# Optimization experiments

Measured on AMD Instinct MI355X. Metric: run time of the kernel, lower is better.

Reference implementation:

```python
import jax, jax.numpy as jnp
import numpy as np


def setup_inputs() -> dict:
    key = jax.random.key(0)
    ks = jax.random.split(key, 5)
    B, T, H, L = 32, 1024, 512, 2
    scale = 1.0 / np.sqrt(H)
    x = jax.random.normal(ks[0], (B, T, H), dtype=jnp.float32)
    Wi = jax.random.normal(ks[1], (L, 4 * H, H), dtype=jnp.float32) * scale
    bi = jax.random.normal(ks[2], (L, 4 * H), dtype=jnp.float32) * scale
    Ws = jax.random.normal(ks[3], (L, 4 * H, H), dtype=jnp.float32) * scale
    # state_linearity bias: zeros except forget slice [H:2H] = 1 (reset_parameters)
    bs = jnp.zeros((L, 4 * H), dtype=jnp.float32)
    bs = bs.at[:, H:2 * H].set(1.0)
    return {"x": x, "Wi": Wi, "bi": bi, "Ws": Ws, "bs": bs}


def reference(x, Wi, bi, Ws, bs):
    # x: [B,T,H]; Wi/Ws: [L,4C,H]; bi/bs: [L,4C]; here C == H (no projection layer)
    B, T, H = x.shape
    L = Wi.shape[0]
    C = H

    def step(carry, x_t):
        h, c = carry  # each [L,B,C]
        inp = x_t  # [B,H]
        new_h, new_c = [], []
        for j in range(L):
            z = inp @ Wi[j].T + bi[j] + h[j] @ Ws[j].T + bs[j]  # [B,4C]
            ig = jax.nn.sigmoid(z[:, 0 * C:1 * C])
            fg = jax.nn.sigmoid(z[:, 1 * C:2 * C])
            gg = jnp.tanh(z[:, 2 * C:3 * C])
            og = jax.nn.sigmoid(z[:, 3 * C:4 * C])
            c_j = ig * gg + fg * c[j]
            h_j = og * jnp.tanh(c_j) + inp  # residual skip connection
            inp = h_j
            new_h.append(h_j)
            new_c.append(c_j)
        return (jnp.stack(new_h), jnp.stack(new_c)), inp

    h0 = jnp.zeros((L, B, C), dtype=x.dtype)
    c0 = jnp.zeros((L, B, C), dtype=x.dtype)
    (h_f, c_f), ys = jax.lax.scan(step, (h0, c0), jnp.swapaxes(x, 0, 1))
    out = jnp.swapaxes(ys, 0, 1)  # [B,T,H]
    # final states as (B, L, H) matching module layout
    return out, jnp.swapaxes(h_f, 0, 1), jnp.swapaxes(c_f, 0, 1)
```

## Files before the change

### kernel.cpp

```cpp
#include <hip/hip_runtime.h>


typedef unsigned int uint32;
typedef unsigned short ushort;

constexpr int B = 32, T = 1024, H = 512, NL = 2;
constexpr int KTOT = 2 * H;
constexpr int BH   = B * H;
constexpr size_t BTH = (size_t)B * T * H;
constexpr size_t BLH = (size_t)B * NL * H;

using bf16x8  = __attribute__((ext_vector_type(8))) short;
using floatx4 = __attribute__((ext_vector_type(4))) float;
using uint4v  = __attribute__((ext_vector_type(4))) uint32;

__device__ __forceinline__ float frcp(float x) { return __builtin_amdgcn_rcpf(x); }
__device__ __forceinline__ float sigm(float v) { return frcp(1.0f + __expf(-v)); }
__device__ __forceinline__ float tanh_fast(float v) {
    return 1.0f - 2.0f * frcp(1.0f + __expf(2.0f * v));
}

__device__ __forceinline__ ushort f2bf(float f) {
    uint32 u = __builtin_bit_cast(uint32, f);
    u += 0x7fffu + ((u >> 16) & 1u);
    return (ushort)(u >> 16);
}

__launch_bounds__(512, 1)
__global__ void lstm_persist(const float* __restrict__ x,
                             const float* __restrict__ Wi,
                             const float* __restrict__ bi,
                             const float* __restrict__ Ws,
                             const float* __restrict__ bs,
                             float* __restrict__ out,
                             uint32* __restrict__ ctrl,
                             uint32* __restrict__ h0pk,
                             uint32* __restrict__ h1pk)
{
    extern __shared__ short smem[];
    short* whi = smem;
    short* wlo = smem + 32 * KTOT;
    float* red = (float*)(smem + 64 * KTOT);

    const int wg    = blockIdx.x;
    const int tid   = threadIdx.x;
    const int layer = wg & 1;
    const int rg    = wg >> 1;
    const int chb   = rg * 8;

    for (int i = tid; i < 32 * KTOT; i += 512) {
        const int n = i >> 10, k = i & (KTOT - 1);
        const int g = n >> 3, c = n & 7;
        const int grow = g * H + chb + c;
        const float v = (k < H) ? Wi[((size_t)layer * 4 * H + grow) * H + k]
                                : Ws[((size_t)layer * 4 * H + grow) * H + (k - H)];
        const ushort hb = f2bf(v);
        const float  hf = __builtin_bit_cast(float, (uint32)hb << 16);
        const ushort lb = f2bf(v - hf);
        const int off = (n * 128 + ((k >> 3) ^ n)) * 8 + (k & 7);
        whi[off] = (short)hb;
        wlo[off] = (short)lb;
    }

    const int lane = tid & 63;
    const int w    = tid >> 6;
    const int mt   = w & 1;
    const int kq   = w >> 1;
    const int quad = lane >> 4;
    const int mrow = lane & 15;
    const int bb   = mt * 16 + mrow;
    const int nn   = mrow;

    const int ec = tid & 7, eb = tid >> 3;
    float cs = 0.f;
    float bias_[4] = {0.f, 0.f, 0.f, 0.f};
    if (tid < 256) {
        #pragma unroll
        for (int g = 0; g < 4; ++g) {
            const int grow = g * H + chb + ec;
            bias_[g] = bi[layer * 4 * H + grow] + bs[layer * 4 * H + grow];
        }
    }

    const bool xwave = (layer == 0) && (kq < 2);
    float4 xq[16];
    if (xwave) {
        const float* xb = x + ((size_t)bb * T + 0) * H + kq * 256 + quad * 8;
        #pragma unroll
        for (int st = 0; st < 8; ++st) {
            xq[2 * st]     = *(const float4*)(xb + st * 32);
            xq[2 * st + 1] = *(const float4*)(xb + st * 32 + 4);
        }
    }
    __syncthreads();

    for (int s = 0; s <= T; ++s) {
        const int t = (layer == 0) ? s : s - 1;
        const bool active = (t >= 0 && t < T);

        float resid = 0.f;
        if (active && tid < 256) {
            const int ch = chb + ec;
            if (layer == 0) {
                resid = x[((size_t)eb * T + t) * H + ch];
            } else {
                const uint32 rp = __hip_atomic_load(
                    &h0pk[(size_t)(t & 1) * BH + (size_t)eb * H + ch],
                    __ATOMIC_RELAXED, __HIP_MEMORY_SCOPE_AGENT);
                resid = __builtin_bit_cast(float, rp << 16)
                      + __builtin_bit_cast(float, rp & 0xffff0000u);
            }
        }

        if (active) {
            floatx4 acc0 = {0.f, 0.f, 0.f, 0.f};
            floatx4 acc1 = {0.f, 0.f, 0.f, 0.f};
            floatx4 acc2 = {0.f, 0.f, 0.f, 0.f};
            floatx4 acc3 = {0.f, 0.f, 0.f, 0.f};

            if (xwave) {
                #pragma unroll
                for (int st = 0; st < 8; ++st) {
                    const float4 f0 = xq[2 * st], f1 = xq[2 * st + 1];
                    const float vv[8] = {f0.x, f0.y, f0.z, f0.w, f1.x, f1.y, f1.z, f1.w};
                    bf16x8 ahi, alo;
                    #pragma unroll
                    for (int j = 0; j < 8; ++j) {
                        const ushort hb = f2bf(vv[j]);
                        const float  hf = __builtin_bit_cast(float, (uint32)hb << 16);
                        ahi[j] = (short)hb;
                        alo[j] = (short)f2bf(vv[j] - hf);
                    }
                    const int cb = kq * 32 + st * 4 + quad;
                    const int n1 = 16 + nn;
                    const int woff0 = (nn * 128 + (cb ^ nn)) * 8;
                    const int woff1 = (n1 * 128 + (cb ^ n1)) * 8;
                    const bf16x8 bh0 = *(const bf16x8*)(whi + woff0);
                    const bf16x8 bl0 = *(const bf16x8*)(wlo + woff0);
                    const bf16x8 bh1 = *(const bf16x8*)(whi + woff1);
                    const bf16x8 bl1 = *(const bf16x8*)(wlo + woff1);
                    acc0 = __builtin_amdgcn_mfma_f32_16x16x32_bf16(ahi, bh0, acc0, 0, 0, 0);
                    acc1 = __builtin_amdgcn_mfma_f32_16x16x32_bf16(alo, bh0, acc1, 0, 0, 0);
                    acc1 = __builtin_amdgcn_mfma_f32_16x16x32_bf16(ahi, bl0, acc1, 0, 0, 0);
                    acc2 = __builtin_amdgcn_mfma_f32_16x16x32_bf16(ahi, bh1, acc2, 0, 0, 0);
                    acc3 = __builtin_amdgcn_mfma_f32_16x16x32_bf16(alo, bh1, acc3, 0, 0, 0);
                    acc3 = __builtin_amdgcn_mfma_f32_16x16x32_bf16(ahi, bl1, acc3, 0, 0, 0);
                }
            } else {
                int par, koff;
                const uint32* hbuf;
                if (layer == 0)   { par = (t - 1) & 1; koff = kq * 256 - 512; hbuf = h0pk; }
                else if (kq < 2)  { par = t & 1;       koff = kq * 256;       hbuf = h0pk; }
                else              { par = (t - 1) & 1; koff = kq * 256 - 512; hbuf = h1pk; }
                const uint32* hp = hbuf + (size_t)par * BH + (size_t)bb * H + koff + quad * 8;

                uint4v q0,q1,q2,q3,q4,q5,q6,q7,q8,q9,q10,q11,q12,q13,q14,q15;
                asm volatile(
                    "global_load_dwordx4 %0,  %16, off sc0 sc1\n\t"
                    "global_load_dwordx4 %1,  %16, off offset:16 sc0 sc1\n\t"
                    "global_load_dwordx4 %2,  %16, off offset:128 sc0 sc1\n\t"
                    "global_load_dwordx4 %3,  %16, off offset:144 sc0 sc1\n\t"
                    "global_load_dwordx4 %4,  %16, off offset:256 sc0 sc1\n\t"
                    "global_load_dwordx4 %5,  %16, off offset:272 sc0 sc1\n\t"
                    "global_load_dwordx4 %6,  %16, off offset:384 sc0 sc1\n\t"
                    "global_load_dwordx4 %7,  %16, off offset:400 sc0 sc1\n\t"
                    "global_load_dwordx4 %8,  %16, off offset:512 sc0 sc1\n\t"
                    "global_load_dwordx4 %9,  %16, off offset:528 sc0 sc1\n\t"
                    "global_load_dwordx4 %10, %16, off offset:640 sc0 sc1\n\t"
                    "global_load_dwordx4 %11, %16, off offset:656 sc0 sc1\n\t"
                    "global_load_dwordx4 %12, %16, off offset:768 sc0 sc1\n\t"
                    "global_load_dwordx4 %13, %16, off offset:784 sc0 sc1\n\t"
                    "global_load_dwordx4 %14, %16, off offset:896 sc0 sc1\n\t"
                    "global_load_dwordx4 %15, %16, off offset:912 sc0 sc1\n\t"
                    "s_waitcnt vmcnt(0)"
                    : "=&v"(q0), "=&v"(q1), "=&v"(q2), "=&v"(q3),
                      "=&v"(q4), "=&v"(q5), "=&v"(q6), "=&v"(q7),
                      "=&v"(q8), "=&v"(q9), "=&v"(q10), "=&v"(q11),
                      "=&v"(q12), "=&v"(q13), "=&v"(q14), "=&v"(q15)
                    : "v"(hp)
                    : "memory");
                const uint4v qq[16] = {q0,q1,q2,q3,q4,q5,q6,q7,q8,q9,q10,q11,q12,q13,q14,q15};

                #pragma unroll
                for (int st = 0; st < 8; ++st) {
                    const uint4v ea = qq[2 * st], eb4 = qq[2 * st + 1];
                    uint4v hiw, low;
                    hiw[0] = __builtin_amdgcn_perm(ea[1],  ea[0],  0x05040100u);
                    hiw[1] = __builtin_amdgcn_perm(ea[3],  ea[2],  0x05040100u);
                    hiw[2] = __builtin_amdgcn_perm(eb4[1], eb4[0], 0x05040100u);
                    hiw[3] = __builtin_amdgcn_perm(eb4[3], eb4[2], 0x05040100u);
                    low[0] = __builtin_amdgcn_perm(ea[1],  ea[0],  0x07060302u);
                    low[1] = __builtin_amdgcn_perm(ea[3],  ea[2],  0x07060302u);
                    low[2] = __builtin_amdgcn_perm(eb4[1], eb4[0], 0x07060302u);
                    low[3] = __builtin_amdgcn_perm(eb4[3], eb4[2], 0x07060302u);
                    const bf16x8 ahi = __builtin_bit_cast(bf16x8, hiw);
                    const bf16x8 alo = __builtin_bit_cast(bf16x8, low);
                    const int cb = kq * 32 + st * 4 + quad;
                    const int n1 = 16 + nn;
                    const int woff0 = (nn * 128 + (cb ^ nn)) * 8;
                    const int woff1 = (n1 * 128 + (cb ^ n1)) * 8;
                    const bf16x8 bh0 = *(const bf16x8*)(whi + woff0);
                    const bf16x8 bl0 = *(const bf16x8*)(wlo + woff0);
                    const bf16x8 bh1 = *(const bf16x8*)(whi + woff1);
                    const bf16x8 bl1 = *(const bf16x8*)(wlo + woff1);
                    acc0 = __builtin_amdgcn_mfma_f32_16x16x32_bf16(ahi, bh0, acc0, 0, 0, 0);
                    acc1 = __builtin_amdgcn_mfma_f32_16x16x32_bf16(alo, bh0, acc1, 0, 0, 0);
                    acc1 = __builtin_amdgcn_mfma_f32_16x16x32_bf16(ahi, bl0, acc1, 0, 0, 0);
                    acc2 = __builtin_amdgcn_mfma_f32_16x16x32_bf16(ahi, bh1, acc2, 0, 0, 0);
                    acc3 = __builtin_amdgcn_mfma_f32_16x16x32_bf16(alo, bh1, acc3, 0, 0, 0);
                    acc3 = __builtin_amdgcn_mfma_f32_16x16x32_bf16(ahi, bl1, acc3, 0, 0, 0);
                }
            }
            floatx4 zr0, zr1;
            zr0[0] = acc0[0] + acc1[0]; zr0[1] = acc0[1] + acc1[1];
            zr0[2] = acc0[2] + acc1[2]; zr0[3] = acc0[3] + acc1[3];
            zr1[0] = acc2[0] + acc3[0]; zr1[1] = acc2[1] + acc3[1];
            zr1[2] = acc2[2] + acc3[2]; zr1[3] = acc2[3] + acc3[3];
            *(floatx4*)&red[((w * 2 + 0) * 64 + lane) * 4] = zr0;
            *(floatx4*)&red[((w * 2 + 1) * 64 + lane) * 4] = zr1;
        }
        __syncthreads();

        float hn_s = 0.f;
        if (active && tid < 256) {
            const int m = eb & 15, emt = eb >> 4, q = m >> 2, r = m & 3;
            const int ch = chb + ec;
            float z[4];
            #pragma unroll
            for (int g = 0; g < 4; ++g) {
                const int n = g * 8 + ec;
                const int nt = n >> 4, col = n & 15;
                const int li = q * 16 + col;
                float a = bias_[g];
                #pragma unroll
                for (int kqe = 0; kqe < 4; ++kqe)
                    a += red[((((kqe * 2 + emt) * 2) + nt) * 64 + li) * 4 + r];
                z[g] = a;
            }
            const float ig = sigm(z[0]), fg = sigm(z[1]);
            const float gg = tanh_fast(z[2]), og = sigm(z[3]);
            cs = ig * gg + fg * cs;
            hn_s = og * tanh_fast(cs) + resid;

            const ushort hb = f2bf(hn_s);
            const float  hf = __builtin_bit_cast(float, (uint32)hb << 16);
            const ushort lb = f2bf(hn_s - hf);
            const uint32 pk = (uint32)hb | ((uint32)lb << 16);
            const size_t hidx = (size_t)(t & 1) * BH + (size_t)eb * H + ch;
            if (layer == 0) {
                __hip_atomic_store(&h0pk[hidx], pk, __ATOMIC_RELAXED, __HIP_MEMORY_SCOPE_AGENT);
            } else {
                __hip_atomic_store(&h1pk[hidx], pk, __ATOMIC_RELAXED, __HIP_MEMORY_SCOPE_AGENT);
            }
        }

        __syncthreads();

        if (tid == 448 && s < T) {
            const uint32 e = (uint32)s + 1u;
            const uint32 rr = __hip_atomic_fetch_add(&ctrl[0], 1u, __ATOMIC_RELAXED,
                                                     __HIP_MEMORY_SCOPE_AGENT);
            if (rr == e * 128u - 1u)
                __hip_atomic_store(&ctrl[512], e,
                                   __ATOMIC_RELAXED, __HIP_MEMORY_SCOPE_AGENT);
        }

        if (active && tid < 256) {
            const int ch = chb + ec;
            if (layer == 1)
                out[((size_t)eb * T + t) * H + ch] = hn_s;
            if (t == T - 1) {
                out[BTH + ((size_t)eb * NL + layer) * H + ch] = hn_s;
                out[BTH + BLH + ((size_t)eb * NL + layer) * H + ch] = cs;
            }
        }

        if (s < T) {
            if (xwave && (s + 1) < T) {
                const float* xb = x + ((size_t)bb * T + (s + 1)) * H + kq * 256 + quad * 8;
                #pragma unroll
                for (int st = 0; st < 8; ++st) {
                    xq[2 * st]     = *(const float4*)(xb + st * 32);
                    xq[2 * st + 1] = *(const float4*)(xb + st * 32 + 4);
                }
            }
            const uint32 e = (uint32)s + 1u;
            if (tid >= 448) {
                const uint32* fp = ctrl + 512;
                for (;;) {
                    uint32 f;
                    asm volatile("global_load_dword %0, %1, off sc0 sc1\n\t"
                                 "s_waitcnt vmcnt(0)"
                                 : "=v"(f) : "v"(fp) : "memory");
                    if (__all(f >= e)) break;
                    __builtin_amdgcn_s_sleep(1);
                }
            }
            __syncthreads();
        }
    }
}

extern "C" void kernel_launch(void* const* d_in, const int* in_sizes, int n_in,
                              void* d_out, int out_size, void* d_ws, size_t ws_size,
                              hipStream_t stream) {
    const float* x  = (const float*)d_in[0];
    const float* Wi = (const float*)d_in[1];
    const float* bi = (const float*)d_in[2];
    const float* Ws = (const float*)d_in[3];
    const float* bs = (const float*)d_in[4];
    float* out = (float*)d_out;

    char* wsb = (char*)d_ws;
    uint32* ctrl = (uint32*)wsb;
    uint32* h0pk = (uint32*)(wsb + 4096);
    uint32* h1pk = (uint32*)(wsb + 4096 + 131072);
    const size_t zero_bytes = 4096 + 2 * 131072;

    static const size_t lds_bytes = (size_t)(64 * KTOT) * sizeof(short)
                                  + (size_t)8 * 2 * 64 * 4 * sizeof(float);
    hipFuncSetAttribute((const void*)lstm_persist,
                        hipFuncAttributeMaxDynamicSharedMemorySize, (int)lds_bytes);

    hipMemsetAsync(d_ws, 0, zero_bytes, stream);
    hipLaunchKernelGGL(lstm_persist, dim3(128), dim3(512), lds_bytes, stream,
                       x, Wi, bi, Ws, bs, out, ctrl, h0pk, h1pk);
}
```

Before: 6.616 ms.

## Split global step barrier into per-layer flags with fine-grained waits

Replaces the single all-workgroup barrier per timestep with separate per-layer arrival counters and replicated flag lines. Each wave now waits only for what it needs: layer-1 waves wait on both layers' flags, layer-0 recurrent waves wait on their own layer, and x-input waves skip the wait, so layer-0 can start its input-side MMA before the recurrent state is ready. The write of layer-0 h is gated on layer-1 having consumed the previous buffer. The goal is to shorten the critical path and let the two layers pipeline. The cost is more polling traffic and subtle ordering requirements on the double-buffered h, which could cause races or deadlock if any wait is wrong.

```diff
diff --git a/kernel.cpp b/kernel.cpp
--- a/kernel.cpp
+++ b/kernel.cpp
@@ -12,6 +12,7 @@
 
 using bf16x8  = __attribute__((ext_vector_type(8))) short;
 using floatx4 = __attribute__((ext_vector_type(4))) float;
+using uint2v  = __attribute__((ext_vector_type(2))) uint32;
 using uint4v  = __attribute__((ext_vector_type(4))) uint32;
 
 __device__ __forceinline__ float frcp(float x) { return __builtin_amdgcn_rcpf(x); }
@@ -82,6 +83,8 @@
         }
     }
 
+    const uint32* fline = ctrl + 512 + (wg & 3) * 32;
+
     const bool xwave = (layer == 0) && (kq < 2);
     float4 xq[16];
     if (xwave) {
@@ -97,6 +100,29 @@
     for (int s = 0; s <= T; ++s) {
         const int t = (layer == 0) ? s : s - 1;
         const bool active = (t >= 0 && t < T);
+        const uint32 eg = (uint32)s;
+
+        if (active && s > 0) {
+            if (layer == 1) {
+                for (;;) {
+                    uint2v f;
+                    asm volatile("global_load_dwordx2 %0, %1, off sc0 sc1\n\t"
+                                 "s_waitcnt vmcnt(0)"
+                                 : "=v"(f) : "v"(fline) : "memory");
+                    if (__all((f[0] >= eg) && (f[1] >= eg))) break;
+                    __builtin_amdgcn_s_sleep(1);
+                }
+            } else if (kq >= 2) {
+                for (;;) {
+                    uint32 f;
+                    asm volatile("global_load_dword %0, %1, off sc0 sc1\n\t"
+                                 "s_waitcnt vmcnt(0)"
+                                 : "=v"(f) : "v"(fline) : "memory");
+                    if (__all(f >= eg)) break;
+                    __builtin_amdgcn_s_sleep(1);
+                }
+            }
+        }
 
         float resid = 0.f;
         if (active && tid < 256) {
@@ -242,6 +268,18 @@
             cs = ig * gg + fg * cs;
             hn_s = og * tanh_fast(cs) + resid;
 
+            if (layer == 0 && s > 0) {
+                const uint32* fl1 = fline + 1;
+                for (;;) {
+                    uint32 f;
+                    asm volatile("global_load_dword %0, %1, off sc0 sc1\n\t"
+                                 "s_waitcnt vmcnt(0)"
+                                 : "=v"(f) : "v"(fl1) : "memory");
+                    if (__all(f >= eg)) break;
+                    __builtin_amdgcn_s_sleep(1);
+                }
+            }
+
             const ushort hb = f2bf(hn_s);
             const float  hf = __builtin_bit_cast(float, (uint32)hb << 16);
             const ushort lb = f2bf(hn_s - hf);
@@ -258,11 +296,15 @@
 
         if (tid == 448 && s < T) {
             const uint32 e = (uint32)s + 1u;
-            const uint32 rr = __hip_atomic_fetch_add(&ctrl[0], 1u, __ATOMIC_RELAXED,
+            uint32* cnt = (layer == 0) ? &ctrl[0] : &ctrl[32];
+            const uint32 rr = __hip_atomic_fetch_add(cnt, 1u, __ATOMIC_RELAXED,
                                                      __HIP_MEMORY_SCOPE_AGENT);
-            if (rr == e * 128u - 1u)
-                __hip_atomic_store(&ctrl[512], e,
-                                   __ATOMIC_RELAXED, __HIP_MEMORY_SCOPE_AGENT);
+            if (rr == e * 64u - 1u) {
+                #pragma unroll
+                for (int r4 = 0; r4 < 4; ++r4)
+                    __hip_atomic_store(&ctrl[512 + layer + r4 * 32], e,
+                                       __ATOMIC_RELAXED, __HIP_MEMORY_SCOPE_AGENT);
+            }
         }
 
         if (active && tid < 256) {
@@ -275,28 +317,13 @@
             }
         }
 
-        if (s < T) {
-            if (xwave && (s + 1) < T) {
-                const float* xb = x + ((size_t)bb * T + (s + 1)) * H + kq * 256 + quad * 8;
-                #pragma unroll
-                for (int st = 0; st < 8; ++st) {
-                    xq[2 * st]     = *(const float4*)(xb + st * 32);
-                    xq[2 * st + 1] = *(const float4*)(xb + st * 32 + 4);
-                }
-            }
-            const uint32 e = (uint32)s + 1u;
-            if (tid >= 448) {
-                const uint32* fp = ctrl + 512;
-                for (;;) {
-                    uint32 f;
-                    asm volatile("global_load_dword %0, %1, off sc0 sc1\n\t"
-                                 "s_waitcnt vmcnt(0)"
-                                 : "=v"(f) : "v"(fp) : "memory");
-                    if (__all(f >= e)) break;
-                    __builtin_amdgcn_s_sleep(1);
-                }
-            }
-            __syncthreads();
+        if (xwave && (s + 1) < T) {
+            const float* xb = x + ((size_t)bb * T + (s + 1)) * H + kq * 256 + quad * 8;
+            #pragma unroll
+            for (int st = 0; st < 8; ++st) {
+                xq[2 * st]     = *(const float4*)(xb + st * 32);
+                xq[2 * st + 1] = *(const float4*)(xb + st * 32 + 4);
+            }
         }
     }
 }
```

Measured after the change: 6.527 ms. No clear change (-1.4%).
